# Performance work log

Measured on AMD Instinct MI355X. Metric: run time of the kernel, lower is better.

Reference implementation:

```python
import jax, jax.numpy as jnp
import numpy as np

NUM_TREE = 64
TREE_DEPTH = 4
NUM_LEAF = 2 ** (TREE_DEPTH + 1)        # 32
NUM_INTERNALS = NUM_LEAF - 1            # 31
IN_DIM = 512
OUT_DIM = 16
BATCH = 8192


def build_route_masks(tree_depth: int, num_internals: int, num_leaf: int) -> np.ndarray:
    """Static gather indices into the [p, 1-p] concatenated prob vector (length 2*num_internals).
    Returns [tree_depth+1, num_leaf]; product over level axis gives leaf path probabilities.
    Mirrors the increment_mask construction in the torch forward."""
    masks = []
    num_repeat = num_leaf // 2
    num_local_internals = 1
    masks.append(np.repeat(np.array([0, num_internals]), num_repeat))
    for _ in range(1, tree_depth + 1):
        num_repeat //= 2
        num_local_internals *= 2
        m = np.repeat(np.arange(num_local_internals - 1, 2 * num_local_internals - 1), 2)
        m = m + np.tile(np.array([0, num_internals]), num_local_internals)
        m = np.repeat(m, num_repeat)
        masks.append(m)
    return np.stack(masks).astype(np.int32)  # [depth+1, num_leaf]


ROUTE_MASKS = jnp.asarray(build_route_masks(TREE_DEPTH, NUM_INTERNALS, NUM_LEAF))


def setup_inputs() -> dict:
    key = jax.random.key(0)
    k1, k2, k3 = jax.random.split(key, 3)
    x = jax.random.normal(k1, (BATCH, IN_DIM), dtype=jnp.float32)
    # xavier-ish scale so sigmoid gates are not saturated
    W = jax.random.normal(k2, (NUM_TREE * NUM_INTERNALS, IN_DIM), dtype=jnp.float32) / np.sqrt(IN_DIM)
    b = jnp.zeros((NUM_TREE * NUM_INTERNALS,), dtype=jnp.float32)
    leafs = jax.random.normal(k3, (NUM_TREE, NUM_LEAF, OUT_DIM), dtype=jnp.float32)
    return {"x": x, "W": W, "b": b, "leafs": leafs}


def reference(x, W, b, leafs) -> jnp.ndarray:
    B = x.shape[0]
    T, L, O = leafs.shape
    I = L - 1
    tree_net = x @ W.T + b                                  # [B, T*I]
    p = jax.nn.sigmoid(tree_net).reshape(B, T, I)           # split per tree
    flat = jnp.concatenate([p, 1.0 - p], axis=-1)           # [B, T, 2I]
    gathered = flat[:, :, ROUTE_MASKS]                      # [B, T, depth+1, L]
    routes = jnp.prod(gathered, axis=2)                     # [B, T, L] leaf path probs
    leafs_sm = jax.nn.softmax(leafs, axis=-1)
    features = routes.reshape(B, T * L)
    out = features @ leafs_sm.reshape(T * L, O) / T
    return out
```

## Files before the change

### kernel.cpp

```cpp
#include <hip/hip_runtime.h>

#define BATCH 8192
#define IN_DIM 512
#define NT 64
#define NI 31
#define NL 32
#define ODIM 16
#define NPAD (NT*NL)
#define NCB 16

typedef __attribute__((ext_vector_type(8))) short bf16x8;
typedef __attribute__((ext_vector_type(4))) float f32x4;

__device__ __forceinline__ unsigned short f2b(float f) {
  union { float f; unsigned int u; } v; v.f = f;
  unsigned int r = v.u + 0x7fffu + ((v.u >> 16) & 1u);
  return (unsigned short)(r >> 16);
}
__device__ __forceinline__ float b2f(unsigned short h) {
  union { unsigned int u; float f; } v; v.u = ((unsigned int)h) << 16;
  return v.f;
}

__global__ __launch_bounds__(256) void prep_kernel(
    const float* __restrict__ x, const float* __restrict__ W,
    const float* __restrict__ leafs,
    unsigned short* __restrict__ xb, unsigned short* __restrict__ wb,
    float* __restrict__ lsm)
{
  const int NXg = BATCH * (IN_DIM/8);
  const int NWg = NPAD  * (IN_DIM/8);
  const int NS  = NT*NL;
  int gid = blockIdx.x*256 + threadIdx.x;
  if (gid < NXg) {
    int row = gid >> 6, k8 = gid & 63;
    int kt = k8 >> 2, g = k8 & 3;
    int gs = g ^ ((row >> 1) & 3);
    const float* s = x + (size_t)row*IN_DIM + kt*32 + gs*8;
    float4 v0 = ((const float4*)s)[0], v1 = ((const float4*)s)[1];
    ushort4 o0, o1;
    o0.x=f2b(v0.x); o0.y=f2b(v0.y); o0.z=f2b(v0.z); o0.w=f2b(v0.w);
    o1.x=f2b(v1.x); o1.y=f2b(v1.y); o1.z=f2b(v1.z); o1.w=f2b(v1.w);
    ((ushort4*)xb)[gid*2]   = o0;
    ((ushort4*)xb)[gid*2+1] = o1;
  } else if ((gid -= NXg) < NWg) {
    int row = gid >> 6, k8 = gid & 63;
    int t = row >> 5, i = row & 31;
    int kt = k8 >> 2, g = k8 & 3;
    int gs = g ^ ((row >> 1) & 3);
    ushort4 o0, o1;
    if (i == 31) { o0.x=o0.y=o0.z=o0.w=0; o1=o0; }
    else {
      const float* s = W + (size_t)(t*NI+i)*IN_DIM + kt*32 + gs*8;
      float4 v0 = ((const float4*)s)[0], v1 = ((const float4*)s)[1];
      o0.x=f2b(v0.x); o0.y=f2b(v0.y); o0.z=f2b(v0.z); o0.w=f2b(v0.w);
      o1.x=f2b(v1.x); o1.y=f2b(v1.y); o1.z=f2b(v1.z); o1.w=f2b(v1.w);
    }
    ((ushort4*)wb)[gid*2]   = o0;
    ((ushort4*)wb)[gid*2+1] = o1;
  } else if ((gid -= NWg) < NS) {
    const float* src = leafs + (size_t)gid*ODIM;
    float m = src[0];
    #pragma unroll
    for (int o=1;o<ODIM;++o) m = fmaxf(m, src[o]);
    float e[ODIM]; float s = 0.f;
    #pragma unroll
    for (int o=0;o<ODIM;++o) { e[o] = __expf(src[o]-m); s += e[o]; }
    float inv = 1.f/(s*(float)NT);
    #pragma unroll
    for (int o=0;o<ODIM;++o) lsm[(size_t)gid*ODIM+o] = e[o]*inv;
  }
}

__device__ __forceinline__ void async16(const unsigned short* g, unsigned short* l) {
  __builtin_amdgcn_global_load_lds(
      (const __attribute__((address_space(1))) unsigned int*)g,
      (__attribute__((address_space(3))) unsigned int*)l,
      16, 0, 0);
}

#define STG 12288

__global__ __launch_bounds__(256, 2) void fused_kernel(
    const unsigned short* __restrict__ xb, const unsigned short* __restrict__ wb,
    const float* __restrict__ bias, const float* __restrict__ lsm,
    float* __restrict__ part)
{
  __shared__ __align__(16) unsigned short smem[34816];

  const int tid  = threadIdx.x;
  const int lane = tid & 63;
  const int wave = tid >> 6;
  const int wm = wave & 1, wn = wave >> 1;

  const int bid = blockIdx.x;
  const int m_t = (bid & 7)*4 + (bid >> 7);
  const int n_t = (bid >> 3) & 15;
  const int m0 = m_t * 256, n0 = n_t * 128;

  f32x4 acc[8][4];
  #pragma unroll
  for (int i=0;i<8;++i)
    #pragma unroll
    for (int j=0;j<4;++j) { f32x4 z = {0.f,0.f,0.f,0.f}; acc[i][j] = z; }

  const int srow = lane >> 2, scol = (lane & 3) * 8;
  const unsigned short* gaw = xb + (size_t)(m0 + wave*64 + srow)*IN_DIM + scol;
  const unsigned short* gbw = wb + (size_t)(n0 + wave*32 + srow)*IN_DIM + scol;

  const int l15 = lane & 15, quad = lane >> 4;
  const int cs   = (quad ^ ((l15 >> 1) & 3)) << 3;

  #pragma unroll
  for (int c=0;c<4;++c) async16(gaw + c*16*IN_DIM, smem + wave*2048 + c*512);
  #pragma unroll
  for (int c=0;c<2;++c) async16(gbw + c*16*IN_DIM, smem + 8192 + wave*1024 + c*512);

  for (int kt = 0; kt < 16; ++kt) {
    __syncthreads();
    const int cur = (kt & 1) * STG;
    if (kt < 15) {
      const int nxt = ((kt + 1) & 1) * STG;
      const int ko = (kt + 1) * 32;
      #pragma unroll
      for (int c=0;c<4;++c)
        async16(gaw + ko + c*16*IN_DIM, smem + nxt + wave*2048 + c*512);
      #pragma unroll
      for (int c=0;c<2;++c)
        async16(gbw + ko + c*16*IN_DIM, smem + nxt + 8192 + wave*1024 + c*512);
    }
    const unsigned short* As = smem + cur;
    const unsigned short* Bs = smem + cur + 8192;
    bf16x8 af[8], bfr[4];
    #pragma unroll
    for (int mi=0;mi<8;++mi)
      af[mi] = *(const bf16x8*)(As + (wm*128 + mi*16 + l15)*32 + cs);
    #pragma unroll
    for (int ni=0;ni<4;++ni)
      bfr[ni] = *(const bf16x8*)(Bs + (wn*64 + ni*16 + l15)*32 + cs);
    #pragma unroll
    for (int mi=0;mi<8;++mi)
      #pragma unroll
      for (int ni=0;ni<4;++ni)
        acc[mi][ni] = __builtin_amdgcn_mfma_f32_16x16x32_bf16(
            af[mi], bfr[ni], acc[mi][ni], 0, 0, 0);
  }

  bf16x8 bleaf[4];
  {
    const int t0 = n_t * 4;
    #pragma unroll
    for (int s=0;s<4;++s) {
      union { bf16x8 v; unsigned short u[8]; } tmp;
      #pragma unroll
      for (int j=0;j<8;++j)
        tmp.u[j] = f2b(lsm[((size_t)(t0+s)*NL + quad*8 + j)*ODIM + l15]);
      bleaf[s] = tmp.v;
    }
  }

  __syncthreads();

  unsigned short* Pt = smem;
  #pragma unroll
  for (int ni=0;ni<4;++ni) {
    int cl = wn*64 + ni*16 + l15;
    int gcol = n0 + cl;
    int tt = gcol >> 5, ii = gcol & 31;
    float bv = (ii < NI) ? bias[tt*NI + ii] : 0.f;
    #pragma unroll
    for (int mi=0;mi<8;++mi) {
      int lrow = wm*128 + mi*16 + quad*4;
      #pragma unroll
      for (int r=0;r<4;++r) {
        float v = acc[mi][ni][r] + bv;
        Pt[(lrow + r)*130 + cl] = f2b(1.f/(1.f + __expf(-v)));
      }
    }
  }
  __syncthreads();

  const int row = tid;
  unsigned int rt[64];
  #pragma unroll
  for (int tl=0; tl<4; ++tl) {
    const unsigned short* pr = Pt + row*130 + tl*32;
    float q[31];
    #pragma unroll
    for (int i=0;i<31;++i) q[i] = b2f(pr[i]);
    float v[32];
    v[0] = q[0]; v[1] = 1.f - q[0];
    #pragma unroll
    for (int d=1; d<=4; ++d) {
      const int s = 1 << d;
      #pragma unroll
      for (int j=s-1; j>=0; --j) {
        float pj = q[(s-1)+j];
        float base = v[j];
        v[2*j]   = base * pj;
        v[2*j+1] = base * (1.f - pj);
      }
    }
    #pragma unroll
    for (int k=0;k<16;++k)
      rt[tl*16+k] = (unsigned int)f2b(v[2*k]) | ((unsigned int)f2b(v[2*k+1]) << 16);
  }
  __syncthreads();

  unsigned int* Rt32 = (unsigned int*)smem;
  {
    uint4* dst = (uint4*)(Rt32 + row*68);
    #pragma unroll
    for (int c=0;c<16;++c) {
      uint4 w; w.x=rt[c*4]; w.y=rt[c*4+1]; w.z=rt[c*4+2]; w.w=rt[c*4+3];
      dst[c] = w;
    }
  }
  __syncthreads();

  const unsigned short* RtS = smem;
  #pragma unroll
  for (int mt=0; mt<4; ++mt) {
    const int mrow = (wave*4 + mt)*16;
    f32x4 a2 = {0.f,0.f,0.f,0.f};
    #pragma unroll
    for (int s=0;s<4;++s) {
      bf16x8 af2 = *(const bf16x8*)(RtS + (mrow + l15)*136 + s*32 + quad*8);
      a2 = __builtin_amdgcn_mfma_f32_16x16x32_bf16(af2, bleaf[s], a2, 0, 0, 0);
    }
    float* op = part + ((size_t)n_t*BATCH + (m0 + mrow + quad*4))*ODIM + l15;
    #pragma unroll
    for (int r=0;r<4;++r)
      op[r*ODIM] = a2[r];
  }
}

__global__ __launch_bounds__(256) void reduce_kernel(
    const float* __restrict__ part, float* __restrict__ out)
{
  int gid = blockIdx.x*256 + threadIdx.x;
  const float4* p4 = (const float4*)part;
  float4 s = p4[gid];
  #pragma unroll
  for (int cb=1; cb<NCB; ++cb) {
    float4 v = p4[(size_t)cb*(BATCH*ODIM/4) + gid];
    s.x+=v.x; s.y+=v.y; s.z+=v.z; s.w+=v.w;
  }
  ((float4*)out)[gid] = s;
}

extern "C" void kernel_launch(void* const* d_in, const int* in_sizes, int n_in,
                              void* d_out, int out_size, void* d_ws, size_t ws_size,
                              hipStream_t stream) {
  const float* x     = (const float*)d_in[0];
  const float* W     = (const float*)d_in[1];
  const float* b     = (const float*)d_in[2];
  const float* leafs = (const float*)d_in[3];
  float* out = (float*)d_out;

  char* ws = (char*)d_ws;
  unsigned short* xb  = (unsigned short*)ws;
  unsigned short* wb  = (unsigned short*)(ws + 8388608);
  float*          lsm = (float*)(ws + 10485760);
  float*          part= (float*)(ws + 10616832);

  const int total = BATCH*(IN_DIM/8) + NPAD*(IN_DIM/8) + NT*NL;
  prep_kernel<<<dim3((total + 255)/256), dim3(256), 0, stream>>>(
      x, W, leafs, xb, wb, lsm);
  fused_kernel<<<dim3(512), dim3(256), 0, stream>>>(
      xb, wb, b, lsm, part);
  reduce_kernel<<<dim3(BATCH*ODIM/4/256), dim3(256), 0, stream>>>(part, out);
}
```

Before: 104.3 us.

## Triple-buffer GEMM k-loop with vmcnt waits, setprio, and vectorized P reads

Moves the main GEMM loop from double to triple buffering. The loop prefetches two k-tiles ahead, waits with a partial s_waitcnt vmcnt instead of a full __syncthreads, and peels the last iteration. It raises wave priority around the MFMA block with s_setprio. It also pads the sigmoid tile row stride to 132 so each row can be read as 8-byte short4 vectors instead of scalar loads. The aim is to hide global-to-LDS latency better and cut LDS read instructions, at the cost of more shared memory per block, which may affect the two-blocks-per-CU occupancy.

```diff
diff --git a/kernel.cpp b/kernel.cpp
--- a/kernel.cpp
+++ b/kernel.cpp
@@ -86,7 +86,7 @@
     const float* __restrict__ bias, const float* __restrict__ lsm,
     float* __restrict__ part)
 {
-  __shared__ __align__(16) unsigned short smem[34816];
+  __shared__ __align__(16) unsigned short smem[36864];
 
   const int tid  = threadIdx.x;
   const int lane = tid & 63;
@@ -112,25 +112,32 @@
   const int cs   = (quad ^ ((l15 >> 1) & 3)) << 3;
 
   #pragma unroll
-  for (int c=0;c<4;++c) async16(gaw + c*16*IN_DIM, smem + wave*2048 + c*512);
-  #pragma unroll
-  for (int c=0;c<2;++c) async16(gbw + c*16*IN_DIM, smem + 8192 + wave*1024 + c*512);
-
-  for (int kt = 0; kt < 16; ++kt) {
-    __syncthreads();
-    const int cur = (kt & 1) * STG;
-    if (kt < 15) {
-      const int nxt = ((kt + 1) & 1) * STG;
-      const int ko = (kt + 1) * 32;
+  for (int c=0;c<4;++c) async16(gaw + c*16*IN_DIM,      smem + wave*2048 + c*512);
+  #pragma unroll
+  for (int c=0;c<2;++c) async16(gbw + c*16*IN_DIM,      smem + 8192 + wave*1024 + c*512);
+  #pragma unroll
+  for (int c=0;c<4;++c) async16(gaw + 32 + c*16*IN_DIM, smem + STG + wave*2048 + c*512);
+  #pragma unroll
+  for (int c=0;c<2;++c) async16(gbw + 32 + c*16*IN_DIM, smem + STG + 8192 + wave*1024 + c*512);
+
+  unsigned short* st0 = smem;
+  unsigned short* st1 = smem + STG;
+  unsigned short* st2 = smem + 2*STG;
+
+  for (int kt = 0; kt < 15; ++kt) {
+    asm volatile("s_waitcnt vmcnt(6)" ::: "memory");
+    __builtin_amdgcn_s_barrier();
+    if (kt < 14) {
+      const int ko = (kt + 2) * 32;
       #pragma unroll
       for (int c=0;c<4;++c)
-        async16(gaw + ko + c*16*IN_DIM, smem + nxt + wave*2048 + c*512);
+        async16(gaw + ko + c*16*IN_DIM, st2 + wave*2048 + c*512);
       #pragma unroll
       for (int c=0;c<2;++c)
-        async16(gbw + ko + c*16*IN_DIM, smem + nxt + 8192 + wave*1024 + c*512);
-    }
-    const unsigned short* As = smem + cur;
-    const unsigned short* Bs = smem + cur + 8192;
+        async16(gbw + ko + c*16*IN_DIM, st2 + 8192 + wave*1024 + c*512);
+    }
+    const unsigned short* As = st0;
+    const unsigned short* Bs = st0 + 8192;
     bf16x8 af[8], bfr[4];
     #pragma unroll
     for (int mi=0;mi<8;++mi)
@@ -138,12 +145,36 @@
     #pragma unroll
     for (int ni=0;ni<4;++ni)
       bfr[ni] = *(const bf16x8*)(Bs + (wn*64 + ni*16 + l15)*32 + cs);
+    __builtin_amdgcn_s_setprio(1);
     #pragma unroll
     for (int mi=0;mi<8;++mi)
       #pragma unroll
       for (int ni=0;ni<4;++ni)
         acc[mi][ni] = __builtin_amdgcn_mfma_f32_16x16x32_bf16(
             af[mi], bfr[ni], acc[mi][ni], 0, 0, 0);
+    __builtin_amdgcn_s_setprio(0);
+    unsigned short* t = st0; st0 = st1; st1 = st2; st2 = t;
+  }
+  asm volatile("s_waitcnt vmcnt(0)" ::: "memory");
+  __builtin_amdgcn_s_barrier();
+  {
+    const unsigned short* As = st0;
+    const unsigned short* Bs = st0 + 8192;
+    bf16x8 af[8], bfr[4];
+    #pragma unroll
+    for (int mi=0;mi<8;++mi)
+      af[mi] = *(const bf16x8*)(As + (wm*128 + mi*16 + l15)*32 + cs);
+    #pragma unroll
+    for (int ni=0;ni<4;++ni)
+      bfr[ni] = *(const bf16x8*)(Bs + (wn*64 + ni*16 + l15)*32 + cs);
+    __builtin_amdgcn_s_setprio(1);
+    #pragma unroll
+    for (int mi=0;mi<8;++mi)
+      #pragma unroll
+      for (int ni=0;ni<4;++ni)
+        acc[mi][ni] = __builtin_amdgcn_mfma_f32_16x16x32_bf16(
+            af[mi], bfr[ni], acc[mi][ni], 0, 0, 0);
+    __builtin_amdgcn_s_setprio(0);
   }
 
   bf16x8 bleaf[4];
@@ -174,7 +205,7 @@
       #pragma unroll
       for (int r=0;r<4;++r) {
         float v = acc[mi][ni][r] + bv;
-        Pt[(lrow + r)*130 + cl] = f2b(1.f/(1.f + __expf(-v)));
+        Pt[(lrow + r)*132 + cl] = f2b(1.f/(1.f + __expf(-v)));
       }
     }
   }
@@ -184,10 +215,13 @@
   unsigned int rt[64];
   #pragma unroll
   for (int tl=0; tl<4; ++tl) {
-    const unsigned short* pr = Pt + row*130 + tl*32;
+    const short4* pr4 = (const short4*)(Pt + row*132 + tl*32);
+    union { short4 v4[8]; unsigned short u[32]; } qb;
+    #pragma unroll
+    for (int c=0;c<8;++c) qb.v4[c] = pr4[c];
     float q[31];
     #pragma unroll
-    for (int i=0;i<31;++i) q[i] = b2f(pr[i]);
+    for (int i=0;i<31;++i) q[i] = b2f(qb.u[i]);
     float v[32];
     v[0] = q[0]; v[1] = 1.f - q[0];
     #pragma unroll
```

After: 103.4 us. About the same (-0.9%).
